# Performance work log

Measured on AMD Instinct MI355X. Metric: run time of the kernel, lower is better.

The kernel has to match this reference:

```python
import jax, jax.numpy as jnp
import numpy as np
from functools import partial

D, H, W = 32, 256, 256   # grid_size (D, H, W)
V = 40000                # number of active voxels
C_IN, C_OUT = 16, 32
K = 3                    # kernel size
P = 32                   # max_points per voxel
EPS = 1e-5               # BatchNorm eps


def setup_inputs() -> dict:
    key = jax.random.key(0)
    k1, k2, k3, k4 = jax.random.split(key, 4)
    voxels = jax.random.normal(k1, (V, C_IN, P), dtype=jnp.float32)
    lin = jax.random.choice(k2, D * H * W, (V,), replace=False)
    d = (lin // (H * W)).astype(jnp.int32)
    h = ((lin // W) % H).astype(jnp.int32)
    w = (lin % W).astype(jnp.int32)
    indices = jnp.stack([w, h, d], axis=1)  # columns are (w, h, d) per original usage
    conv_w = jax.random.normal(k3, (C_OUT, C_IN, K, K, K), dtype=jnp.float32) * 0.05
    conv_b = jax.random.normal(k4, (C_OUT,), dtype=jnp.float32) * 0.05
    gamma = jnp.ones((C_OUT,), dtype=jnp.float32)
    beta = jnp.zeros((C_OUT,), dtype=jnp.float32)
    return {"voxels": voxels, "indices": indices, "conv_w": conv_w,
            "conv_b": conv_b, "gamma": gamma, "beta": beta, "batch_size": 1}


def reference(voxels, indices, conv_w, conv_b, gamma, beta, batch_size):
    # voxel features: mean over points  [V, C]
    feats = voxels.mean(axis=2)
    w_i, h_i, d_i = indices[:, 0], indices[:, 1], indices[:, 2]
    # original: batch_mask = indices[:,0] >= 0, plus per-dim bounds check
    valid = ((w_i >= 0) & (w_i < W) & (h_i >= 0) & (h_i < H) & (d_i >= 0) & (d_i < D))
    d_s = jnp.where(valid, d_i, D)  # route invalid rows out-of-bounds -> dropped
    # fused scatter replacing the python per-voxel loop; [D, H, W, C]
    grid = jnp.zeros((D, H, W, C_IN), dtype=voxels.dtype).at[d_s, h_i, w_i].set(
        feats, mode="drop")
    # same scatter is written into every batch slice in the original
    dense = jnp.broadcast_to(jnp.transpose(grid, (3, 0, 1, 2))[None],
                             (batch_size, C_IN, D, H, W))
    # Conv3d, padding = K//2 (SAME)
    out = jax.lax.conv_general_dilated(
        dense, conv_w, window_strides=(1, 1, 1), padding=[(K // 2, K // 2)] * 3,
        dimension_numbers=("NCDHW", "OIDHW", "NCDHW"))
    out = out + conv_b[None, :, None, None, None]
    # BatchNorm3d (training-mode batch statistics, biased variance)
    mean = out.mean(axis=(0, 2, 3, 4), keepdims=True)
    var = out.var(axis=(0, 2, 3, 4), keepdims=True)
    out = (out - mean) * jax.lax.rsqrt(var + EPS)
    out = out * gamma[None, :, None, None, None] + beta[None, :, None, None, None]
    return jax.nn.relu(out)
```

## Files before the change

kernel.cpp:

```cpp
#include <hip/hip_runtime.h>

#define D_   32
#define H_   256
#define W_   256
#define HW_  (H_ * W_)
#define DHW_ (D_ * H_ * W_)
#define V_   40000
#define CIN  16
#define COUT 32
#define P_   32
#define EPS_ 1e-5f

#define TD 2
#define TH 8
#define TW 32
#define NTX (W_ / TW)
#define NTY (H_ / TH)
#define NTZ (D_ / TD)
#define NT  (NTX * NTY * NTZ)
#define TPOS (TD * TH * TW)
#define OH 8
#define NQ (COUT / OH)
#define TROW 9
#define TCT 512
#define SSLOT 64
#define TAPC 640
#define WTN  (NQ * 27 * 4 * OH)
#define WTBLK ((WTN + 255) / 256)
#define CBLK  (V_ * 8 / 256)
#define FPBLK (V_ * CIN / 256)

__global__ void prep_kernel(const int* __restrict__ idxs, int* __restrict__ tapcnt,
                            const float* __restrict__ conv_w, float4* __restrict__ wt4,
                            const float* __restrict__ vox, float* __restrict__ feats) {
    int b = blockIdx.x;
    int t = threadIdx.x;
    if (b < CBLK) {
        int idx = b * 256 + t;
        int v = idx >> 3, r = idx & 7;
        int w = idxs[3 * v], h = idxs[3 * v + 1], d = idxs[3 * v + 2];
        if (!((unsigned)w < W_ && (unsigned)h < H_ && (unsigned)d < D_)) return;
        int dlo = max(d - 1, 0), dhi = min(d + 1, D_ - 1);
        int hlo = max(h - 1, 0), hhi = min(h + 1, H_ - 1);
        int wlo = max(w - 1, 0), whi = min(w + 1, W_ - 1);
        int tz = dlo / TD + ((r >> 2) & 1);
        int ty = hlo / TH + ((r >> 1) & 1);
        int tx = wlo / TW + (r & 1);
        if (tz > dhi / TD || ty > hhi / TH || tx > whi / TW) return;
        int zl = max(dlo, tz * TD), zh = min(dhi, tz * TD + TD - 1);
        int yl = max(hlo, ty * TH), yh = min(hhi, ty * TH + TH - 1);
        int xl = max(wlo, tx * TW), xh = min(whi, tx * TW + TW - 1);
        int cnt = (zh - zl + 1) * (yh - yl + 1) * (xh - xl + 1);
        atomicAdd(&tapcnt[tz * NTY * NTX + ty * NTX + tx], cnt);
        return;
    }
    b -= CBLK;
    if (b < WTBLK) {
        int n = b * 256 + t;
        if (n < WTN) {
            int oo = n & 7;
            int jj = (n >> 3) & 3;
            int m  = n >> 5;
            int k  = m % 27;
            int quarter = m / 27;
            int o = quarter * OH + oo;
            float4 wv;
            wv.x = conv_w[(o * CIN + 4 * jj + 0) * 27 + k];
            wv.y = conv_w[(o * CIN + 4 * jj + 1) * 27 + k];
            wv.z = conv_w[(o * CIN + 4 * jj + 2) * 27 + k];
            wv.w = conv_w[(o * CIN + 4 * jj + 3) * 27 + k];
            wt4[n] = wv;
        }
        return;
    }
    b -= WTBLK;
    int idx = b * 256 + t;
    const float4* p = (const float4*)(vox + (size_t)idx * P_);
    float s = 0.f;
#pragma unroll
    for (int j = 0; j < P_ / 4; ++j) {
        float4 tv = p[j];
        s += tv.x + tv.y + tv.z + tv.w;
    }
    feats[idx] = s * (1.0f / (float)P_);
}

__global__ void scan_kernel(const int* __restrict__ counts, int* __restrict__ starts,
                            int* __restrict__ cursor) {
    __shared__ int part[256];
    int t = threadIdx.x;
    int base = t * 16;
    int s = 0;
    for (int j = 0; j < 16; ++j) s += counts[base + j];
    part[t] = s;
    __syncthreads();
    for (int off = 1; off < 256; off <<= 1) {
        int val = part[t];
        int add = (t >= off) ? part[t - off] : 0;
        __syncthreads();
        part[t] = val + add;
        __syncthreads();
    }
    int run = (t > 0) ? part[t - 1] : 0;
    for (int j = 0; j < 16; ++j) {
        starts[base + j] = run;
        cursor[base + j] = run;
        run += counts[base + j];
    }
}

__global__ void tap_fill_kernel(const int* __restrict__ idxs, int* __restrict__ cursor,
                                int* __restrict__ tapbuf) {
    int idx = blockIdx.x * 256 + threadIdx.x;
    int v = idx >> 3, r = idx & 7;
    int w = idxs[3 * v], h = idxs[3 * v + 1], d = idxs[3 * v + 2];
    if (!((unsigned)w < W_ && (unsigned)h < H_ && (unsigned)d < D_)) return;
    int dlo = max(d - 1, 0), dhi = min(d + 1, D_ - 1);
    int hlo = max(h - 1, 0), hhi = min(h + 1, H_ - 1);
    int wlo = max(w - 1, 0), whi = min(w + 1, W_ - 1);
    int tz = dlo / TD + ((r >> 2) & 1);
    int ty = hlo / TH + ((r >> 1) & 1);
    int tx = wlo / TW + (r & 1);
    if (tz > dhi / TD || ty > hhi / TH || tx > whi / TW) return;
    int zl = max(dlo, tz * TD), zh = min(dhi, tz * TD + TD - 1);
    int yl = max(hlo, ty * TH), yh = min(hhi, ty * TH + TH - 1);
    int xl = max(wlo, tx * TW), xh = min(whi, tx * TW + TW - 1);
    int cnt = (zh - zl + 1) * (yh - yl + 1) * (xh - xl + 1);
    int p = atomicAdd(&cursor[tz * NTY * NTX + ty * NTX + tx], cnt);
    for (int dq = zl; dq <= zh; ++dq)
        for (int hq = yl; hq <= yh; ++hq)
            for (int wq = xl; wq <= xh; ++wq) {
                int k = ((d - dq + 1) * 3 + (h - hq + 1)) * 3 + (w - wq + 1);
                int pos = ((dq & (TD - 1)) * TH + (hq & (TH - 1))) * TW + (wq & (TW - 1));
                tapbuf[p++] = (v << 14) | (k << 9) | pos;
            }
}

__global__ void __launch_bounds__(TCT, 8) tile_conv_kernel(
    const float4* __restrict__ feats4, const float4* __restrict__ wt4,
    const int* __restrict__ tapstart, const int* __restrict__ tapcnt,
    const int* __restrict__ tapbuf, float* __restrict__ stats,
    float* __restrict__ out)
{
    __shared__ float  tile[TPOS * TROW];
    __shared__ float4 wsm4[27 * 4 * OH];
    __shared__ int    taps_l[TAPC];
    __shared__ int    taps_s[TAPC];
    __shared__ int    khist[32];
    __shared__ float  wsum[8][OH], wsq[8][OH];

    int t = threadIdx.x;
    int tile_id = blockIdx.x;
    int gs = tapstart[tile_id];
    int nt = tapcnt[tile_id];
    int tx = tile_id % NTX, ty = (tile_id / NTX) % NTY, tz = tile_id / (NTX * NTY);
    int w0 = tx * TW, h0 = ty * TH, d0 = tz * TD;
    int sl = tile_id & (SSLOT - 1);

    int ntl = min(nt, TAPC);
    if (t < 32) khist[t] = 0;
    for (int j = t; j < ntl; j += TCT) taps_l[j] = tapbuf[gs + j];
    __syncthreads();
    for (int j = t; j < ntl; j += TCT)
        atomicAdd(&khist[(taps_l[j] >> 9) & 31], 1);
    __syncthreads();
    if (t < 64) {
        int x = (t < 27) ? khist[t] : 0;
        int orig = x;
#pragma unroll
        for (int off = 1; off < 32; off <<= 1) {
            int y = __shfl_up(x, off);
            if (t >= off) x += y;
        }
        if (t < 27) khist[t] = x - orig;
    }
    __syncthreads();
    for (int j = t; j < ntl; j += TCT) {
        int tap = taps_l[j];
        int p = atomicAdd(&khist[(tap >> 9) & 31], 1);
        taps_s[p] = tap;
    }
    __syncthreads();

    int oo = t & 7, slot = t >> 3;
    int wave = t >> 6, lane = t & 63;
    int wl = t & 31, rem = t >> 5;
    size_t outb = (size_t)(d0 + (rem >> 3)) * HW_ + (size_t)(h0 + (rem & 7)) * W_
                + (size_t)(w0 + wl);
    int posD = (rem * TW + wl) * TROW;

#pragma unroll
    for (int qq = 0; qq < NQ; ++qq) {
        int obase = qq * OH;
        for (int j = t; j < TPOS * TROW / 4; j += TCT)
            ((float4*)tile)[j] = make_float4(0, 0, 0, 0);
        for (int j = t; j < 27 * 4 * OH; j += TCT)
            wsm4[j] = wt4[qq * (27 * 4 * OH) + j];
        __syncthreads();

        for (int j = slot; j < nt; j += 64) {
            unsigned tap = (unsigned)((j < TAPC) ? taps_s[j] : tapbuf[gs + j]);
            int pos = tap & 511;
            int k = (tap >> 9) & 31;
            int src = tap >> 14;
            const float4* fp = feats4 + (size_t)src * 4;
            float4 f0 = fp[0], f1 = fp[1], f2 = fp[2], f3 = fp[3];
            const float4* wp = &wsm4[k * 32 + oo];
            float4 q0 = wp[0], q1 = wp[8], q2 = wp[16], q3 = wp[24];
            float acc = q0.x * f0.x + q0.y * f0.y + q0.z * f0.z + q0.w * f0.w
                      + q1.x * f1.x + q1.y * f1.y + q1.z * f1.z + q1.w * f1.w
                      + q2.x * f2.x + q2.y * f2.y + q2.z * f2.z + q2.w * f2.w
                      + q3.x * f3.x + q3.y * f3.y + q3.z * f3.z + q3.w * f3.w;
            atomicAdd(&tile[pos * TROW + oo], acc);
        }
        __syncthreads();

        float s1 = 0.f, s2 = 0.f;
        for (int p = slot; p < TPOS; p += 64) {
            float sv = tile[p * TROW + oo];
            s1 += sv;
            s2 += sv * sv;
        }
        s1 += __shfl_xor(s1, 8);  s2 += __shfl_xor(s2, 8);
        s1 += __shfl_xor(s1, 16); s2 += __shfl_xor(s2, 16);
        s1 += __shfl_xor(s1, 32); s2 += __shfl_xor(s2, 32);
        if (lane < OH) { wsum[wave][lane] = s1; wsq[wave][lane] = s2; }

#pragma unroll
        for (int i = 0; i < OH; ++i)
            out[(size_t)(obase + i) * DHW_ + outb] = tile[posD + i];
        __syncthreads();

        if (t < OH) {
            float a = 0.f, b = 0.f;
#pragma unroll
            for (int wv = 0; wv < 8; ++wv) { a += wsum[wv][t]; b += wsq[wv][t]; }
            atomicAdd(&stats[(obase + t) * SSLOT + sl], a);
            atomicAdd(&stats[COUT * SSLOT + (obase + t) * SSLOT + sl], b);
        }
    }
}

__global__ void finalize_kernel(const float* __restrict__ stats,
                                const float* __restrict__ gamma,
                                const float* __restrict__ beta,
                                float* __restrict__ mi) {
    int t = threadIdx.x;
    if (t < COUT) {
        float m1 = 0.f, m2 = 0.f;
#pragma unroll 8
        for (int s = 0; s < SSLOT; ++s) {
            m1 += stats[t * SSLOT + s];
            m2 += stats[COUT * SSLOT + t * SSLOT + s];
        }
        float n = (float)DHW_;
        m1 /= n;
        m2 /= n;
        float var = fmaxf(m2 - m1 * m1, 0.f);
        float inv = rsqrtf(var + EPS_);
        float A = gamma[t] * inv;
        mi[t] = A;
        mi[COUT + t] = -m1 * A + beta[t];
    }
}

__global__ void __launch_bounds__(256) norm_kernel(float* __restrict__ out,
                                                   const float* __restrict__ mi) {
    int bid = blockIdx.x;
    int c = bid >> 9;
    float A = mi[c], B = mi[COUT + c];
    float4* o4 = (float4*)out;
    int base = bid * 1024 + threadIdx.x;
    float4 x0 = o4[base];
    float4 x1 = o4[base + 256];
    float4 x2 = o4[base + 512];
    float4 x3 = o4[base + 768];
    x0.x = fmaxf(fmaf(x0.x, A, B), 0.f); x0.y = fmaxf(fmaf(x0.y, A, B), 0.f);
    x0.z = fmaxf(fmaf(x0.z, A, B), 0.f); x0.w = fmaxf(fmaf(x0.w, A, B), 0.f);
    x1.x = fmaxf(fmaf(x1.x, A, B), 0.f); x1.y = fmaxf(fmaf(x1.y, A, B), 0.f);
    x1.z = fmaxf(fmaf(x1.z, A, B), 0.f); x1.w = fmaxf(fmaf(x1.w, A, B), 0.f);
    x2.x = fmaxf(fmaf(x2.x, A, B), 0.f); x2.y = fmaxf(fmaf(x2.y, A, B), 0.f);
    x2.z = fmaxf(fmaf(x2.z, A, B), 0.f); x2.w = fmaxf(fmaf(x2.w, A, B), 0.f);
    x3.x = fmaxf(fmaf(x3.x, A, B), 0.f); x3.y = fmaxf(fmaf(x3.y, A, B), 0.f);
    x3.z = fmaxf(fmaf(x3.z, A, B), 0.f); x3.w = fmaxf(fmaf(x3.w, A, B), 0.f);
    o4[base]       = x0;
    o4[base + 256] = x1;
    o4[base + 512] = x2;
    o4[base + 768] = x3;
}

extern "C" void kernel_launch(void* const* d_in, const int* in_sizes, int n_in,
                              void* d_out, int out_size, void* d_ws, size_t ws_size,
                              hipStream_t stream) {
    const float* voxels  = (const float*)d_in[0];
    const int*   indices = (const int*)  d_in[1];
    const float* conv_w  = (const float*)d_in[2];
    const float* gamma   = (const float*)d_in[4];
    const float* beta    = (const float*)d_in[5];
    float* out = (float*)d_out;

    float4* wt4      = (float4*)d_ws;
    float*  stats    = (float*)(wt4 + WTN);
    float*  mi       = stats + 2 * COUT * SSLOT;
    int*    tapcnt   = (int*)(mi + 2 * COUT);
    int*    tapstart = tapcnt + NT;
    int*    tapcur   = tapstart + NT;
    float*  feats    = (float*)(tapcur + NT);
    int*    tapbuf   = (int*)(feats + (size_t)V_ * CIN);

    hipMemsetAsync(stats, 0, 2 * COUT * SSLOT * sizeof(float), stream);
    hipMemsetAsync(tapcnt, 0, NT * sizeof(int), stream);

    prep_kernel<<<CBLK + WTBLK + FPBLK, 256, 0, stream>>>(indices, tapcnt, conv_w, wt4,
                                                          voxels, feats);
    scan_kernel<<<1, 256, 0, stream>>>(tapcnt, tapstart, tapcur);
    tap_fill_kernel<<<CBLK, 256, 0, stream>>>(indices, tapcur, tapbuf);

    tile_conv_kernel<<<NT, TCT, 0, stream>>>((const float4*)feats, wt4, tapstart, tapcnt,
                                             tapbuf, stats, out);

    finalize_kernel<<<1, 64, 0, stream>>>(stats, gamma, beta, mi);
    norm_kernel<<<COUT * 512, 256, 0, stream>>>(out, mi);
}
```

Measured before the change: 643.4 us.

## Fuse all stages into one persistent kernel with global atomic barriers

Replaces the six separate launches and two memsets with a single persistent kernel of 1024 blocks that runs every stage and separates them with a hand-rolled grid barrier (atomic counter plus spin-wait). The tile convolution loops over tiles per block, and the normalization pass is folded in as a grid-strided tail. The aim is to remove launch overhead and inter-kernel gaps. In exchange it relies on all 1024 blocks of 512 threads being co-resident, or the barrier deadlocks. It also gives up the per-kernel occupancy tuning and the LDS staging of taps through taps_l.

```diff
diff --git a/kernel.cpp b/kernel.cpp
--- a/kernel.cpp
+++ b/kernel.cpp
@@ -26,227 +26,234 @@
 #define SSLOT 64
 #define TAPC 640
 #define WTN  (NQ * 27 * 4 * OH)
-#define WTBLK ((WTN + 255) / 256)
-#define CBLK  (V_ * 8 / 256)
-#define FPBLK (V_ * CIN / 256)
-
-__global__ void prep_kernel(const int* __restrict__ idxs, int* __restrict__ tapcnt,
-                            const float* __restrict__ conv_w, float4* __restrict__ wt4,
-                            const float* __restrict__ vox, float* __restrict__ feats) {
-    int b = blockIdx.x;
-    int t = threadIdx.x;
-    if (b < CBLK) {
-        int idx = b * 256 + t;
-        int v = idx >> 3, r = idx & 7;
-        int w = idxs[3 * v], h = idxs[3 * v + 1], d = idxs[3 * v + 2];
-        if (!((unsigned)w < W_ && (unsigned)h < H_ && (unsigned)d < D_)) return;
-        int dlo = max(d - 1, 0), dhi = min(d + 1, D_ - 1);
-        int hlo = max(h - 1, 0), hhi = min(h + 1, H_ - 1);
-        int wlo = max(w - 1, 0), whi = min(w + 1, W_ - 1);
-        int tz = dlo / TD + ((r >> 2) & 1);
-        int ty = hlo / TH + ((r >> 1) & 1);
-        int tx = wlo / TW + (r & 1);
-        if (tz > dhi / TD || ty > hhi / TH || tx > whi / TW) return;
-        int zl = max(dlo, tz * TD), zh = min(dhi, tz * TD + TD - 1);
-        int yl = max(hlo, ty * TH), yh = min(hhi, ty * TH + TH - 1);
-        int xl = max(wlo, tx * TW), xh = min(whi, tx * TW + TW - 1);
-        int cnt = (zh - zl + 1) * (yh - yl + 1) * (xh - xl + 1);
-        atomicAdd(&tapcnt[tz * NTY * NTX + ty * NTX + tx], cnt);
-        return;
-    }
-    b -= CBLK;
-    if (b < WTBLK) {
-        int n = b * 256 + t;
-        if (n < WTN) {
-            int oo = n & 7;
-            int jj = (n >> 3) & 3;
-            int m  = n >> 5;
-            int k  = m % 27;
-            int quarter = m / 27;
-            int o = quarter * OH + oo;
-            float4 wv;
-            wv.x = conv_w[(o * CIN + 4 * jj + 0) * 27 + k];
-            wv.y = conv_w[(o * CIN + 4 * jj + 1) * 27 + k];
-            wv.z = conv_w[(o * CIN + 4 * jj + 2) * 27 + k];
-            wv.w = conv_w[(o * CIN + 4 * jj + 3) * 27 + k];
-            wt4[n] = wv;
-        }
-        return;
-    }
-    b -= WTBLK;
-    int idx = b * 256 + t;
-    const float4* p = (const float4*)(vox + (size_t)idx * P_);
-    float s = 0.f;
-#pragma unroll
-    for (int j = 0; j < P_ / 4; ++j) {
-        float4 tv = p[j];
-        s += tv.x + tv.y + tv.z + tv.w;
-    }
-    feats[idx] = s * (1.0f / (float)P_);
+#define NBLK 1024
+
+__device__ __forceinline__ void gbar(int* bar, int target) {
+    __syncthreads();
+    if (threadIdx.x == 0) {
+        __threadfence();
+        atomicAdd(bar, 1);
+        while (__hip_atomic_load(bar, __ATOMIC_RELAXED, __HIP_MEMORY_SCOPE_AGENT) < target)
+            __builtin_amdgcn_s_sleep(32);
+        __threadfence();
+    }
+    __syncthreads();
 }
 
-__global__ void scan_kernel(const int* __restrict__ counts, int* __restrict__ starts,
-                            int* __restrict__ cursor) {
-    __shared__ int part[256];
-    int t = threadIdx.x;
-    int base = t * 16;
-    int s = 0;
-    for (int j = 0; j < 16; ++j) s += counts[base + j];
-    part[t] = s;
-    __syncthreads();
-    for (int off = 1; off < 256; off <<= 1) {
-        int val = part[t];
-        int add = (t >= off) ? part[t - off] : 0;
-        __syncthreads();
-        part[t] = val + add;
-        __syncthreads();
-    }
-    int run = (t > 0) ? part[t - 1] : 0;
-    for (int j = 0; j < 16; ++j) {
-        starts[base + j] = run;
-        cursor[base + j] = run;
-        run += counts[base + j];
-    }
-}
-
-__global__ void tap_fill_kernel(const int* __restrict__ idxs, int* __restrict__ cursor,
-                                int* __restrict__ tapbuf) {
-    int idx = blockIdx.x * 256 + threadIdx.x;
-    int v = idx >> 3, r = idx & 7;
-    int w = idxs[3 * v], h = idxs[3 * v + 1], d = idxs[3 * v + 2];
-    if (!((unsigned)w < W_ && (unsigned)h < H_ && (unsigned)d < D_)) return;
-    int dlo = max(d - 1, 0), dhi = min(d + 1, D_ - 1);
-    int hlo = max(h - 1, 0), hhi = min(h + 1, H_ - 1);
-    int wlo = max(w - 1, 0), whi = min(w + 1, W_ - 1);
-    int tz = dlo / TD + ((r >> 2) & 1);
-    int ty = hlo / TH + ((r >> 1) & 1);
-    int tx = wlo / TW + (r & 1);
-    if (tz > dhi / TD || ty > hhi / TH || tx > whi / TW) return;
-    int zl = max(dlo, tz * TD), zh = min(dhi, tz * TD + TD - 1);
-    int yl = max(hlo, ty * TH), yh = min(hhi, ty * TH + TH - 1);
-    int xl = max(wlo, tx * TW), xh = min(whi, tx * TW + TW - 1);
-    int cnt = (zh - zl + 1) * (yh - yl + 1) * (xh - xl + 1);
-    int p = atomicAdd(&cursor[tz * NTY * NTX + ty * NTX + tx], cnt);
-    for (int dq = zl; dq <= zh; ++dq)
-        for (int hq = yl; hq <= yh; ++hq)
-            for (int wq = xl; wq <= xh; ++wq) {
-                int k = ((d - dq + 1) * 3 + (h - hq + 1)) * 3 + (w - wq + 1);
-                int pos = ((dq & (TD - 1)) * TH + (hq & (TH - 1))) * TW + (wq & (TW - 1));
-                tapbuf[p++] = (v << 14) | (k << 9) | pos;
-            }
-}
-
-__global__ void __launch_bounds__(TCT, 8) tile_conv_kernel(
-    const float4* __restrict__ feats4, const float4* __restrict__ wt4,
-    const int* __restrict__ tapstart, const int* __restrict__ tapcnt,
-    const int* __restrict__ tapbuf, float* __restrict__ stats,
-    float* __restrict__ out)
+__global__ void __launch_bounds__(TCT, 8) mega_kernel(
+    const int* __restrict__ idxs, const float* __restrict__ conv_w,
+    const float* __restrict__ vox, const float* __restrict__ gamma,
+    const float* __restrict__ beta, float* __restrict__ out,
+    float4* __restrict__ wt4, float* __restrict__ stats, float* __restrict__ mi,
+    int* __restrict__ tapcnt, int* __restrict__ tapstart, int* __restrict__ tapcur,
+    float* __restrict__ feats, int* __restrict__ tapbuf, int* __restrict__ bar)
 {
     __shared__ float  tile[TPOS * TROW];
     __shared__ float4 wsm4[27 * 4 * OH];
-    __shared__ int    taps_l[TAPC];
     __shared__ int    taps_s[TAPC];
     __shared__ int    khist[32];
     __shared__ float  wsum[8][OH], wsq[8][OH];
-
-    int t = threadIdx.x;
-    int tile_id = blockIdx.x;
-    int gs = tapstart[tile_id];
-    int nt = tapcnt[tile_id];
-    int tx = tile_id % NTX, ty = (tile_id / NTX) % NTY, tz = tile_id / (NTX * NTY);
-    int w0 = tx * TW, h0 = ty * TH, d0 = tz * TD;
-    int sl = tile_id & (SSLOT - 1);
-
-    int ntl = min(nt, TAPC);
-    if (t < 32) khist[t] = 0;
-    for (int j = t; j < ntl; j += TCT) taps_l[j] = tapbuf[gs + j];
-    __syncthreads();
-    for (int j = t; j < ntl; j += TCT)
-        atomicAdd(&khist[(taps_l[j] >> 9) & 31], 1);
-    __syncthreads();
-    if (t < 64) {
-        int x = (t < 27) ? khist[t] : 0;
-        int orig = x;
-#pragma unroll
-        for (int off = 1; off < 32; off <<= 1) {
-            int y = __shfl_up(x, off);
-            if (t >= off) x += y;
-        }
-        if (t < 27) khist[t] = x - orig;
-    }
-    __syncthreads();
-    for (int j = t; j < ntl; j += TCT) {
-        int tap = taps_l[j];
-        int p = atomicAdd(&khist[(tap >> 9) & 31], 1);
-        taps_s[p] = tap;
-    }
-    __syncthreads();
-
-    int oo = t & 7, slot = t >> 3;
-    int wave = t >> 6, lane = t & 63;
-    int wl = t & 31, rem = t >> 5;
-    size_t outb = (size_t)(d0 + (rem >> 3)) * HW_ + (size_t)(h0 + (rem & 7)) * W_
-                + (size_t)(w0 + wl);
-    int posD = (rem * TW + wl) * TROW;
-
-#pragma unroll
-    for (int qq = 0; qq < NQ; ++qq) {
-        int obase = qq * OH;
-        for (int j = t; j < TPOS * TROW / 4; j += TCT)
-            ((float4*)tile)[j] = make_float4(0, 0, 0, 0);
-        for (int j = t; j < 27 * 4 * OH; j += TCT)
-            wsm4[j] = wt4[qq * (27 * 4 * OH) + j];
-        __syncthreads();
-
-        for (int j = slot; j < nt; j += 64) {
-            unsigned tap = (unsigned)((j < TAPC) ? taps_s[j] : tapbuf[gs + j]);
-            int pos = tap & 511;
-            int k = (tap >> 9) & 31;
-            int src = tap >> 14;
-            const float4* fp = feats4 + (size_t)src * 4;
-            float4 f0 = fp[0], f1 = fp[1], f2 = fp[2], f3 = fp[3];
-            const float4* wp = &wsm4[k * 32 + oo];
-            float4 q0 = wp[0], q1 = wp[8], q2 = wp[16], q3 = wp[24];
-            float acc = q0.x * f0.x + q0.y * f0.y + q0.z * f0.z + q0.w * f0.w
-                      + q1.x * f1.x + q1.y * f1.y + q1.z * f1.z + q1.w * f1.w
-                      + q2.x * f2.x + q2.y * f2.y + q2.z * f2.z + q2.w * f2.w
-                      + q3.x * f3.x + q3.y * f3.y + q3.z * f3.z + q3.w * f3.w;
-            atomicAdd(&tile[pos * TROW + oo], acc);
-        }
-        __syncthreads();
-
-        float s1 = 0.f, s2 = 0.f;
-        for (int p = slot; p < TPOS; p += 64) {
-            float sv = tile[p * TROW + oo];
-            s1 += sv;
-            s2 += sv * sv;
-        }
-        s1 += __shfl_xor(s1, 8);  s2 += __shfl_xor(s2, 8);
-        s1 += __shfl_xor(s1, 16); s2 += __shfl_xor(s2, 16);
-        s1 += __shfl_xor(s1, 32); s2 += __shfl_xor(s2, 32);
-        if (lane < OH) { wsum[wave][lane] = s1; wsq[wave][lane] = s2; }
-
-#pragma unroll
-        for (int i = 0; i < OH; ++i)
-            out[(size_t)(obase + i) * DHW_ + outb] = tile[posD + i];
-        __syncthreads();
-
-        if (t < OH) {
-            float a = 0.f, b = 0.f;
-#pragma unroll
-            for (int wv = 0; wv < 8; ++wv) { a += wsum[wv][t]; b += wsq[wv][t]; }
-            atomicAdd(&stats[(obase + t) * SSLOT + sl], a);
-            atomicAdd(&stats[COUT * SSLOT + (obase + t) * SSLOT + sl], b);
-        }
-    }
-}
-
-__global__ void finalize_kernel(const float* __restrict__ stats,
-                                const float* __restrict__ gamma,
-                                const float* __restrict__ beta,
-                                float* __restrict__ mi) {
-    int t = threadIdx.x;
-    if (t < COUT) {
+    __shared__ int    part[256];
+
+    int b = blockIdx.x, t = threadIdx.x;
+    int gid = b * TCT + t;
+
+    if (gid < NT) tapcnt[gid] = 0;
+    else if (gid < NT + 2 * COUT * SSLOT) stats[gid - NT] = 0.f;
+    else if (gid < NT + 2 * COUT * SSLOT + WTN) {
+        int n = gid - NT - 2 * COUT * SSLOT;
+        int oo = n & 7, jj = (n >> 3) & 3;
+        int m = n >> 5, k = m % 27, quarter = m / 27;
+        int o = quarter * OH + oo;
+        float4 wv;
+        wv.x = conv_w[(o * CIN + 4 * jj + 0) * 27 + k];
+        wv.y = conv_w[(o * CIN + 4 * jj + 1) * 27 + k];
+        wv.z = conv_w[(o * CIN + 4 * jj + 2) * 27 + k];
+        wv.w = conv_w[(o * CIN + 4 * jj + 3) * 27 + k];
+        wt4[n] = wv;
+    }
+    for (int idx = gid; idx < V_ * CIN; idx += NBLK * TCT) {
+        const float4* p = (const float4*)(vox + (size_t)idx * P_);
+        float s = 0.f;
+#pragma unroll
+        for (int j = 0; j < P_ / 4; ++j) {
+            float4 tv = p[j];
+            s += tv.x + tv.y + tv.z + tv.w;
+        }
+        feats[idx] = s * (1.0f / (float)P_);
+    }
+    gbar(bar, NBLK);
+
+    if (gid < V_ * 8) {
+        int v = gid >> 3, r = gid & 7;
+        int w = idxs[3 * v], h = idxs[3 * v + 1], d = idxs[3 * v + 2];
+        if ((unsigned)w < W_ && (unsigned)h < H_ && (unsigned)d < D_) {
+            int dlo = max(d - 1, 0), dhi = min(d + 1, D_ - 1);
+            int hlo = max(h - 1, 0), hhi = min(h + 1, H_ - 1);
+            int wlo = max(w - 1, 0), whi = min(w + 1, W_ - 1);
+            int tz = dlo / TD + ((r >> 2) & 1);
+            int ty = hlo / TH + ((r >> 1) & 1);
+            int tx = wlo / TW + (r & 1);
+            if (tz <= dhi / TD && ty <= hhi / TH && tx <= whi / TW) {
+                int zl = max(dlo, tz * TD), zh = min(dhi, tz * TD + TD - 1);
+                int yl = max(hlo, ty * TH), yh = min(hhi, ty * TH + TH - 1);
+                int xl = max(wlo, tx * TW), xh = min(whi, tx * TW + TW - 1);
+                int cnt = (zh - zl + 1) * (yh - yl + 1) * (xh - xl + 1);
+                atomicAdd(&tapcnt[tz * NTY * NTX + ty * NTX + tx], cnt);
+            }
+        }
+    }
+    gbar(bar, 2 * NBLK);
+
+    if (b == 0) {
+        int s = 0;
+        if (t < 256) {
+            int base = t * 16;
+            for (int j = 0; j < 16; ++j) s += tapcnt[base + j];
+            part[t] = s;
+        }
+        __syncthreads();
+        for (int off = 1; off < 256; off <<= 1) {
+            int val = 0, add = 0;
+            if (t < 256) { val = part[t]; add = (t >= off) ? part[t - off] : 0; }
+            __syncthreads();
+            if (t < 256) part[t] = val + add;
+            __syncthreads();
+        }
+        if (t < 256) {
+            int base = t * 16;
+            int run = (t > 0) ? part[t - 1] : 0;
+            for (int j = 0; j < 16; ++j) {
+                tapstart[base + j] = run;
+                tapcur[base + j] = run;
+                run += tapcnt[base + j];
+            }
+        }
+    }
+    gbar(bar, 3 * NBLK);
+
+    if (gid < V_ * 8) {
+        int v = gid >> 3, r = gid & 7;
+        int w = idxs[3 * v], h = idxs[3 * v + 1], d = idxs[3 * v + 2];
+        if ((unsigned)w < W_ && (unsigned)h < H_ && (unsigned)d < D_) {
+            int dlo = max(d - 1, 0), dhi = min(d + 1, D_ - 1);
+            int hlo = max(h - 1, 0), hhi = min(h + 1, H_ - 1);
+            int wlo = max(w - 1, 0), whi = min(w + 1, W_ - 1);
+            int tz = dlo / TD + ((r >> 2) & 1);
+            int ty = hlo / TH + ((r >> 1) & 1);
+            int tx = wlo / TW + (r & 1);
+            if (tz <= dhi / TD && ty <= hhi / TH && tx <= whi / TW) {
+                int zl = max(dlo, tz * TD), zh = min(dhi, tz * TD + TD - 1);
+                int yl = max(hlo, ty * TH), yh = min(hhi, ty * TH + TH - 1);
+                int xl = max(wlo, tx * TW), xh = min(whi, tx * TW + TW - 1);
+                int cnt = (zh - zl + 1) * (yh - yl + 1) * (xh - xl + 1);
+                int p = atomicAdd(&tapcur[tz * NTY * NTX + ty * NTX + tx], cnt);
+                for (int dq = zl; dq <= zh; ++dq)
+                    for (int hq = yl; hq <= yh; ++hq)
+                        for (int wq = xl; wq <= xh; ++wq) {
+                            int k = ((d - dq + 1) * 3 + (h - hq + 1)) * 3 + (w - wq + 1);
+                            int pos = ((dq & (TD - 1)) * TH + (hq & (TH - 1))) * TW
+                                    + (wq & (TW - 1));
+                            tapbuf[p++] = (v << 14) | (k << 9) | pos;
+                        }
+            }
+        }
+    }
+    gbar(bar, 4 * NBLK);
+
+    const float4* feats4 = (const float4*)feats;
+    for (int tile_id = b; tile_id < NT; tile_id += NBLK) {
+        int gs = tapstart[tile_id];
+        int nt = tapcnt[tile_id];
+        int tx = tile_id % NTX, ty = (tile_id / NTX) % NTY, tz = tile_id / (NTX * NTY);
+        int w0 = tx * TW, h0 = ty * TH, d0 = tz * TD;
+        int sl = tile_id & (SSLOT - 1);
+        int ntl = min(nt, TAPC);
+
+        if (t < 32) khist[t] = 0;
+        __syncthreads();
+        for (int j = t; j < ntl; j += TCT)
+            atomicAdd(&khist[(tapbuf[gs + j] >> 9) & 31], 1);
+        __syncthreads();
+        if (t < 64) {
+            int x = (t < 27) ? khist[t] : 0;
+            int orig = x;
+#pragma unroll
+            for (int off = 1; off < 32; off <<= 1) {
+                int y = __shfl_up(x, off);
+                if (t >= off) x += y;
+            }
+            if (t < 27) khist[t] = x - orig;
+        }
+        __syncthreads();
+        for (int j = t; j < ntl; j += TCT) {
+            int tap = tapbuf[gs + j];
+            int p = atomicAdd(&khist[(tap >> 9) & 31], 1);
+            taps_s[p] = tap;
+        }
+        __syncthreads();
+
+        int oo = t & 7, slot = t >> 3;
+        int wave = t >> 6, lane = t & 63;
+        int wl = t & 31, rem = t >> 5;
+        size_t outb = (size_t)(d0 + (rem >> 3)) * HW_ + (size_t)(h0 + (rem & 7)) * W_
+                    + (size_t)(w0 + wl);
+        int posD = (rem * TW + wl) * TROW;
+
+#pragma unroll
+        for (int qq = 0; qq < NQ; ++qq) {
+            int obase = qq * OH;
+            for (int j = t; j < TPOS * TROW / 4; j += TCT)
+                ((float4*)tile)[j] = make_float4(0, 0, 0, 0);
+            for (int j = t; j < 27 * 4 * OH; j += TCT)
+                wsm4[j] = wt4[qq * (27 * 4 * OH) + j];
+            __syncthreads();
+
+            for (int j = slot; j < nt; j += 64) {
+                unsigned tap = (unsigned)((j < TAPC) ? taps_s[j] : tapbuf[gs + j]);
+                int pos = tap & 511;
+                int k = (tap >> 9) & 31;
+                int src = tap >> 14;
+                const float4* fp = feats4 + (size_t)src * 4;
+                float4 f0 = fp[0], f1 = fp[1], f2 = fp[2], f3 = fp[3];
+                const float4* wp = &wsm4[k * 32 + oo];
+                float4 q0 = wp[0], q1 = wp[8], q2 = wp[16], q3 = wp[24];
+                float acc = q0.x * f0.x + q0.y * f0.y + q0.z * f0.z + q0.w * f0.w
+                          + q1.x * f1.x + q1.y * f1.y + q1.z * f1.z + q1.w * f1.w
+                          + q2.x * f2.x + q2.y * f2.y + q2.z * f2.z + q2.w * f2.w
+                          + q3.x * f3.x + q3.y * f3.y + q3.z * f3.z + q3.w * f3.w;
+                atomicAdd(&tile[pos * TROW + oo], acc);
+            }
+            __syncthreads();
+
+            float s1 = 0.f, s2 = 0.f;
+            for (int p = slot; p < TPOS; p += 64) {
+                float sv = tile[p * TROW + oo];
+                s1 += sv;
+                s2 += sv * sv;
+            }
+            s1 += __shfl_xor(s1, 8);  s2 += __shfl_xor(s2, 8);
+            s1 += __shfl_xor(s1, 16); s2 += __shfl_xor(s2, 16);
+            s1 += __shfl_xor(s1, 32); s2 += __shfl_xor(s2, 32);
+            if (lane < OH) { wsum[wave][lane] = s1; wsq[wave][lane] = s2; }
+
+#pragma unroll
+            for (int i = 0; i < OH; ++i)
+                out[(size_t)(obase + i) * DHW_ + outb] = tile[posD + i];
+            __syncthreads();
+
+            if (t < OH) {
+                float a = 0.f, bb = 0.f;
+#pragma unroll
+                for (int wv = 0; wv < 8; ++wv) { a += wsum[wv][t]; bb += wsq[wv][t]; }
+                atomicAdd(&stats[(obase + t) * SSLOT + sl], a);
+                atomicAdd(&stats[COUT * SSLOT + (obase + t) * SSLOT + sl], bb);
+            }
+        }
+    }
+    gbar(bar, 5 * NBLK);
+
+    if (b == 0 && t < COUT) {
         float m1 = 0.f, m2 = 0.f;
 #pragma unroll 8
         for (int s = 0; s < SSLOT; ++s) {
@@ -262,31 +269,33 @@
         mi[t] = A;
         mi[COUT + t] = -m1 * A + beta[t];
     }
-}
-
-__global__ void __launch_bounds__(256) norm_kernel(float* __restrict__ out,
-                                                   const float* __restrict__ mi) {
-    int bid = blockIdx.x;
-    int c = bid >> 9;
-    float A = mi[c], B = mi[COUT + c];
-    float4* o4 = (float4*)out;
-    int base = bid * 1024 + threadIdx.x;
-    float4 x0 = o4[base];
-    float4 x1 = o4[base + 256];
-    float4 x2 = o4[base + 512];
-    float4 x3 = o4[base + 768];
-    x0.x = fmaxf(fmaf(x0.x, A, B), 0.f); x0.y = fmaxf(fmaf(x0.y, A, B), 0.f);
-    x0.z = fmaxf(fmaf(x0.z, A, B), 0.f); x0.w = fmaxf(fmaf(x0.w, A, B), 0.f);
-    x1.x = fmaxf(fmaf(x1.x, A, B), 0.f); x1.y = fmaxf(fmaf(x1.y, A, B), 0.f);
-    x1.z = fmaxf(fmaf(x1.z, A, B), 0.f); x1.w = fmaxf(fmaf(x1.w, A, B), 0.f);
-    x2.x = fmaxf(fmaf(x2.x, A, B), 0.f); x2.y = fmaxf(fmaf(x2.y, A, B), 0.f);
-    x2.z = fmaxf(fmaf(x2.z, A, B), 0.f); x2.w = fmaxf(fmaf(x2.w, A, B), 0.f);
-    x3.x = fmaxf(fmaf(x3.x, A, B), 0.f); x3.y = fmaxf(fmaf(x3.y, A, B), 0.f);
-    x3.z = fmaxf(fmaf(x3.z, A, B), 0.f); x3.w = fmaxf(fmaf(x3.w, A, B), 0.f);
-    o4[base]       = x0;
-    o4[base + 256] = x1;
-    o4[base + 512] = x2;
-    o4[base + 768] = x3;
+    gbar(bar, 6 * NBLK);
+
+    {
+        int c = b >> 5;
+        float A = mi[c], B = mi[COUT + c];
+        float4* o4 = (float4*)out;
+        int base = c * (DHW_ / 4) + (b & 31) * 16384 + t;
+#pragma unroll 2
+        for (int i = 0; i < 32; i += 4) {
+            float4 x0 = o4[base + (i + 0) * 512];
+            float4 x1 = o4[base + (i + 1) * 512];
+            float4 x2 = o4[base + (i + 2) * 512];
+            float4 x3 = o4[base + (i + 3) * 512];
+            x0.x = fmaxf(fmaf(x0.x, A, B), 0.f); x0.y = fmaxf(fmaf(x0.y, A, B), 0.f);
+            x0.z = fmaxf(fmaf(x0.z, A, B), 0.f); x0.w = fmaxf(fmaf(x0.w, A, B), 0.f);
+            x1.x = fmaxf(fmaf(x1.x, A, B), 0.f); x1.y = fmaxf(fmaf(x1.y, A, B), 0.f);
+            x1.z = fmaxf(fmaf(x1.z, A, B), 0.f); x1.w = fmaxf(fmaf(x1.w, A, B), 0.f);
+            x2.x = fmaxf(fmaf(x2.x, A, B), 0.f); x2.y = fmaxf(fmaf(x2.y, A, B), 0.f);
+            x2.z = fmaxf(fmaf(x2.z, A, B), 0.f); x2.w = fmaxf(fmaf(x2.w, A, B), 0.f);
+            x3.x = fmaxf(fmaf(x3.x, A, B), 0.f); x3.y = fmaxf(fmaf(x3.y, A, B), 0.f);
+            x3.z = fmaxf(fmaf(x3.z, A, B), 0.f); x3.w = fmaxf(fmaf(x3.w, A, B), 0.f);
+            o4[base + (i + 0) * 512] = x0;
+            o4[base + (i + 1) * 512] = x1;
+            o4[base + (i + 2) * 512] = x2;
+            o4[base + (i + 3) * 512] = x3;
+        }
+    }
 }
 
 extern "C" void kernel_launch(void* const* d_in, const int* in_sizes, int n_in,
@@ -302,23 +311,16 @@
     float4* wt4      = (float4*)d_ws;
     float*  stats    = (float*)(wt4 + WTN);
     float*  mi       = stats + 2 * COUT * SSLOT;
-    int*    tapcnt   = (int*)(mi + 2 * COUT);
+    int*    bar      = (int*)(mi + 2 * COUT);
+    int*    tapcnt   = bar + 64;
     int*    tapstart = tapcnt + NT;
     int*    tapcur   = tapstart + NT;
     float*  feats    = (float*)(tapcur + NT);
     int*    tapbuf   = (int*)(feats + (size_t)V_ * CIN);
 
-    hipMemsetAsync(stats, 0, 2 * COUT * SSLOT * sizeof(float), stream);
-    hipMemsetAsync(tapcnt, 0, NT * sizeof(int), stream);
-
-    prep_kernel<<<CBLK + WTBLK + FPBLK, 256, 0, stream>>>(indices, tapcnt, conv_w, wt4,
-                                                          voxels, feats);
-    scan_kernel<<<1, 256, 0, stream>>>(tapcnt, tapstart, tapcur);
-    tap_fill_kernel<<<CBLK, 256, 0, stream>>>(indices, tapcur, tapbuf);
-
-    tile_conv_kernel<<<NT, TCT, 0, stream>>>((const float4*)feats, wt4, tapstart, tapcnt,
-                                             tapbuf, stats, out);
-
-    finalize_kernel<<<1, 64, 0, stream>>>(stats, gamma, beta, mi);
-    norm_kernel<<<COUT * 512, 256, 0, stream>>>(out, mi);
+    hipMemsetAsync(bar, 0, sizeof(int), stream);
+
+    mega_kernel<<<NBLK, TCT, 0, stream>>>(indices, conv_w, voxels, gamma, beta, out,
+                                          wt4, stats, mi, tapcnt, tapstart, tapcur,
+                                          feats, tapbuf, bar);
 }
```

After: 1.278 ms. +98.6%, slower.

## Recompute sparse conv in a second pass to fuse BatchNorm+ReLU into output write

Applied to the files above, without the earlier changes.

The conv kernel is split into two launches. The first accumulates only the per-channel sum and sum-of-squares statistics and writes nothing to the dense output. After finalize, a second launch recomputes the same tiled sparse convolution and writes the normalized, ReLU'd values directly. This drops the separate norm pass and the extra full read and write of the large dense output tensor. The cost is doing the tap sorting, tile zeroing and atomic accumulation twice, and a float atomic order that may differ slightly between the two passes.

```diff
diff --git a/kernel.cpp b/kernel.cpp
--- a/kernel.cpp
+++ b/kernel.cpp
@@ -136,11 +136,10 @@
             }
 }
 
-__global__ void __launch_bounds__(TCT, 8) tile_conv_kernel(
+__global__ void __launch_bounds__(TCT, 8) conv_stats_kernel(
     const float4* __restrict__ feats4, const float4* __restrict__ wt4,
     const int* __restrict__ tapstart, const int* __restrict__ tapcnt,
-    const int* __restrict__ tapbuf, float* __restrict__ stats,
-    float* __restrict__ out)
+    const int* __restrict__ tapbuf, float* __restrict__ stats)
 {
     __shared__ float  tile[TPOS * TROW];
     __shared__ float4 wsm4[27 * 4 * OH];
@@ -153,8 +152,6 @@
     int tile_id = blockIdx.x;
     int gs = tapstart[tile_id];
     int nt = tapcnt[tile_id];
-    int tx = tile_id % NTX, ty = (tile_id / NTX) % NTY, tz = tile_id / (NTX * NTY);
-    int w0 = tx * TW, h0 = ty * TH, d0 = tz * TD;
     int sl = tile_id & (SSLOT - 1);
 
     int ntl = min(nt, TAPC);
@@ -184,10 +181,6 @@
 
     int oo = t & 7, slot = t >> 3;
     int wave = t >> 6, lane = t & 63;
-    int wl = t & 31, rem = t >> 5;
-    size_t outb = (size_t)(d0 + (rem >> 3)) * HW_ + (size_t)(h0 + (rem & 7)) * W_
-                + (size_t)(w0 + wl);
-    int posD = (rem * TW + wl) * TROW;
 
 #pragma unroll
     for (int qq = 0; qq < NQ; ++qq) {
@@ -225,10 +218,6 @@
         s1 += __shfl_xor(s1, 16); s2 += __shfl_xor(s2, 16);
         s1 += __shfl_xor(s1, 32); s2 += __shfl_xor(s2, 32);
         if (lane < OH) { wsum[wave][lane] = s1; wsq[wave][lane] = s2; }
-
-#pragma unroll
-        for (int i = 0; i < OH; ++i)
-            out[(size_t)(obase + i) * DHW_ + outb] = tile[posD + i];
         __syncthreads();
 
         if (t < OH) {
@@ -238,6 +227,7 @@
             atomicAdd(&stats[(obase + t) * SSLOT + sl], a);
             atomicAdd(&stats[COUT * SSLOT + (obase + t) * SSLOT + sl], b);
         }
+        __syncthreads();
     }
 }
 
@@ -264,29 +254,90 @@
     }
 }
 
-__global__ void __launch_bounds__(256) norm_kernel(float* __restrict__ out,
-                                                   const float* __restrict__ mi) {
-    int bid = blockIdx.x;
-    int c = bid >> 9;
-    float A = mi[c], B = mi[COUT + c];
-    float4* o4 = (float4*)out;
-    int base = bid * 1024 + threadIdx.x;
-    float4 x0 = o4[base];
-    float4 x1 = o4[base + 256];
-    float4 x2 = o4[base + 512];
-    float4 x3 = o4[base + 768];
-    x0.x = fmaxf(fmaf(x0.x, A, B), 0.f); x0.y = fmaxf(fmaf(x0.y, A, B), 0.f);
-    x0.z = fmaxf(fmaf(x0.z, A, B), 0.f); x0.w = fmaxf(fmaf(x0.w, A, B), 0.f);
-    x1.x = fmaxf(fmaf(x1.x, A, B), 0.f); x1.y = fmaxf(fmaf(x1.y, A, B), 0.f);
-    x1.z = fmaxf(fmaf(x1.z, A, B), 0.f); x1.w = fmaxf(fmaf(x1.w, A, B), 0.f);
-    x2.x = fmaxf(fmaf(x2.x, A, B), 0.f); x2.y = fmaxf(fmaf(x2.y, A, B), 0.f);
-    x2.z = fmaxf(fmaf(x2.z, A, B), 0.f); x2.w = fmaxf(fmaf(x2.w, A, B), 0.f);
-    x3.x = fmaxf(fmaf(x3.x, A, B), 0.f); x3.y = fmaxf(fmaf(x3.y, A, B), 0.f);
-    x3.z = fmaxf(fmaf(x3.z, A, B), 0.f); x3.w = fmaxf(fmaf(x3.w, A, B), 0.f);
-    o4[base]       = x0;
-    o4[base + 256] = x1;
-    o4[base + 512] = x2;
-    o4[base + 768] = x3;
+__global__ void __launch_bounds__(TCT, 8) conv_write_kernel(
+    const float4* __restrict__ feats4, const float4* __restrict__ wt4,
+    const int* __restrict__ tapstart, const int* __restrict__ tapcnt,
+    const int* __restrict__ tapbuf, const float* __restrict__ mi,
+    float* __restrict__ out)
+{
+    __shared__ float  tile[TPOS * TROW];
+    __shared__ float4 wsm4[27 * 4 * OH];
+    __shared__ int    taps_l[TAPC];
+    __shared__ int    taps_s[TAPC];
+    __shared__ int    khist[32];
+
+    int t = threadIdx.x;
+    int tile_id = blockIdx.x;
+    int gs = tapstart[tile_id];
+    int nt = tapcnt[tile_id];
+    int tx = tile_id % NTX, ty = (tile_id / NTX) % NTY, tz = tile_id / (NTX * NTY);
+    int w0 = tx * TW, h0 = ty * TH, d0 = tz * TD;
+
+    int ntl = min(nt, TAPC);
+    if (t < 32) khist[t] = 0;
+    for (int j = t; j < ntl; j += TCT) taps_l[j] = tapbuf[gs + j];
+    __syncthreads();
+    for (int j = t; j < ntl; j += TCT)
+        atomicAdd(&khist[(taps_l[j] >> 9) & 31], 1);
+    __syncthreads();
+    if (t < 64) {
+        int x = (t < 27) ? khist[t] : 0;
+        int orig = x;
+#pragma unroll
+        for (int off = 1; off < 32; off <<= 1) {
+            int y = __shfl_up(x, off);
+            if (t >= off) x += y;
+        }
+        if (t < 27) khist[t] = x - orig;
+    }
+    __syncthreads();
+    for (int j = t; j < ntl; j += TCT) {
+        int tap = taps_l[j];
+        int p = atomicAdd(&khist[(tap >> 9) & 31], 1);
+        taps_s[p] = tap;
+    }
+    __syncthreads();
+
+    int oo = t & 7, slot = t >> 3;
+    int wl = t & 31, rem = t >> 5;
+    size_t outb = (size_t)(d0 + (rem >> 3)) * HW_ + (size_t)(h0 + (rem & 7)) * W_
+                + (size_t)(w0 + wl);
+    int posD = (rem * TW + wl) * TROW;
+
+#pragma unroll
+    for (int qq = 0; qq < NQ; ++qq) {
+        int obase = qq * OH;
+        for (int j = t; j < TPOS * TROW / 4; j += TCT)
+            ((float4*)tile)[j] = make_float4(0, 0, 0, 0);
+        for (int j = t; j < 27 * 4 * OH; j += TCT)
+            wsm4[j] = wt4[qq * (27 * 4 * OH) + j];
+        __syncthreads();
+
+        for (int j = slot; j < nt; j += 64) {
+            unsigned tap = (unsigned)((j < TAPC) ? taps_s[j] : tapbuf[gs + j]);
+            int pos = tap & 511;
+            int k = (tap >> 9) & 31;
+            int src = tap >> 14;
+            const float4* fp = feats4 + (size_t)src * 4;
+            float4 f0 = fp[0], f1 = fp[1], f2 = fp[2], f3 = fp[3];
+            const float4* wp = &wsm4[k * 32 + oo];
+            float4 q0 = wp[0], q1 = wp[8], q2 = wp[16], q3 = wp[24];
+            float acc = q0.x * f0.x + q0.y * f0.y + q0.z * f0.z + q0.w * f0.w
+                      + q1.x * f1.x + q1.y * f1.y + q1.z * f1.z + q1.w * f1.w
+                      + q2.x * f2.x + q2.y * f2.y + q2.z * f2.z + q2.w * f2.w
+                      + q3.x * f3.x + q3.y * f3.y + q3.z * f3.z + q3.w * f3.w;
+            atomicAdd(&tile[pos * TROW + oo], acc);
+        }
+        __syncthreads();
+
+#pragma unroll
+        for (int i = 0; i < OH; ++i) {
+            float A = mi[obase + i], B = mi[COUT + obase + i];
+            out[(size_t)(obase + i) * DHW_ + outb] =
+                fmaxf(fmaf(tile[posD + i], A, B), 0.f);
+        }
+        __syncthreads();
+    }
 }
 
 extern "C" void kernel_launch(void* const* d_in, const int* in_sizes, int n_in,
@@ -316,9 +367,9 @@
     scan_kernel<<<1, 256, 0, stream>>>(tapcnt, tapstart, tapcur);
     tap_fill_kernel<<<CBLK, 256, 0, stream>>>(indices, tapcur, tapbuf);
 
-    tile_conv_kernel<<<NT, TCT, 0, stream>>>((const float4*)feats, wt4, tapstart, tapcnt,
-                                             tapbuf, stats, out);
-
+    conv_stats_kernel<<<NT, TCT, 0, stream>>>((const float4*)feats, wt4, tapstart,
+                                              tapcnt, tapbuf, stats);
     finalize_kernel<<<1, 64, 0, stream>>>(stats, gamma, beta, mi);
-    norm_kernel<<<COUT * 512, 256, 0, stream>>>(out, mi);
-}
+    conv_write_kernel<<<NT, TCT, 0, stream>>>((const float4*)feats, wt4, tapstart,
+                                              tapcnt, tapbuf, mi, out);
+}
```

Result: slower. 796.7 us (+23.8%).
